# Performance work log

Hardware: AMD Instinct MI355X
Metric: run time of the kernel (lower is better)

## Reference

```python
import jax, jax.numpy as jnp
import numpy as np

N = 20000
E = 320000
F_IN = 512
F_OUT = 512
DIFF_T = 1.0
NUM_STEPS = 5
TIME_DECAY = 0.1
LN_EPS = 1e-5


def setup_inputs() -> dict:
    key = jax.random.key(0)
    k_x, k_e, k_ts, k_wt, k_wr = jax.random.split(key, 5)
    x = jax.random.normal(k_x, (N, F_IN), dtype=jnp.float32)
    edge_index = jax.random.randint(k_e, (2, E), 0, N)
    timestamps = jax.random.uniform(k_ts, (E,), dtype=jnp.float32) * 100.0
    lim = float(np.sqrt(6.0 / (F_IN + F_OUT)))  # xavier_uniform
    W_t = jax.random.uniform(k_wt, (F_OUT, F_IN), jnp.float32, -lim, lim)
    b_t = jnp.zeros((F_OUT,), jnp.float32)
    W_r = jax.random.uniform(k_wr, (F_OUT, F_IN), jnp.float32, -lim, lim)
    gamma = jnp.ones((F_OUT,), jnp.float32)
    beta = jnp.zeros((F_OUT,), jnp.float32)
    return {"node_features": x, "edge_index": edge_index, "timestamps": timestamps,
            "W_t": W_t, "b_t": b_t, "W_r": W_r, "gamma": gamma, "beta": beta,
            "graph_time": 100}


def reference(node_features, edge_index, timestamps, W_t, b_t, W_r, gamma, beta, graph_time):
    x = node_features
    n = x.shape[0]
    # append self-loops with timestamp == graph.time
    loop = jnp.arange(n)
    ei = jnp.concatenate([edge_index, jnp.stack([loop, loop], axis=0)], axis=1)
    ts = jnp.concatenate([timestamps, jnp.full((n,), graph_time, jnp.float32)])
    src, dst = ei[0], ei[1]
    # time-decayed symmetric-normalized adjacency weights
    w = jnp.exp(-TIME_DECAY * (ts.max() - ts))  # [E+N]
    deg = jax.ops.segment_sum(w, dst, num_segments=n)  # [N]
    dinv = jnp.where(deg > 0, deg ** -0.5, 0.0)
    ew = dinv[src] * w * dinv[dst]  # [E+N]
    # K Euler steps of heat diffusion: h <- h + dt*(A_norm h - h)
    dt = DIFF_T / NUM_STEPS
    h = x
    for _ in range(NUM_STEPS):
        diffused = jax.ops.segment_sum(ew[:, None] * h[src], dst, num_segments=n)  # [N, F]
        h = h + dt * (diffused - h)
    # transform + residual + layernorm (dropout omitted: eval mode)
    out = jax.nn.relu(h @ W_t.T + b_t) + x @ W_r.T  # [N, F_OUT]
    mu = out.mean(axis=-1, keepdims=True)
    var = out.var(axis=-1, keepdims=True)
    out = (out - mu) * jax.lax.rsqrt(var + LN_EPS) * gamma + beta
    return out
```

## Files before the change

kernel.cpp:

```cpp
#include <hip/hip_runtime.h>
#include <hip/hip_fp16.h>

#define FDIM 512
#define TDK  0.1f
#define DTs  0.2f
#define EPSv 1e-5f

using bf16x8  = __attribute__((ext_vector_type(8))) __bf16;
using floatx4 = __attribute__((ext_vector_type(4))) float;
using ushort8 = __attribute__((ext_vector_type(8))) unsigned short;
using uintx4  = __attribute__((ext_vector_type(4))) unsigned int;

__device__ __forceinline__ unsigned short f2bf(float f) {
  unsigned int u = __float_as_uint(f);
  u += 0x7fffu + ((u >> 16) & 1u);
  return (unsigned short)(u >> 16);
}

__device__ __forceinline__ void gld16(const __bf16* g, __bf16* l) {
  __builtin_amdgcn_global_load_lds(
      (const __attribute__((address_space(1))) unsigned int*)g,
      (__attribute__((address_space(3))) unsigned int*)l, 16, 0, 0);
}

__global__ __launch_bounds__(256) void tsmax_kernel(const float* __restrict__ ts, int E,
                                                    float* __restrict__ out) {
  float m = 0.f;
  for (int i = blockIdx.x * blockDim.x + threadIdx.x; i < E; i += gridDim.x * blockDim.x)
    m = fmaxf(m, ts[i]);
  for (int off = 32; off; off >>= 1) m = fmaxf(m, __shfl_down(m, off));
  __shared__ float sm[4];
  int wid = threadIdx.x >> 6, lane = threadIdx.x & 63;
  if (lane == 0) sm[wid] = m;
  __syncthreads();
  if (threadIdx.x == 0) {
    float mm = fmaxf(fmaxf(sm[0], sm[1]), fmaxf(sm[2], sm[3]));
    atomicMax((int*)out, __float_as_int(mm));
  }
}

__global__ __launch_bounds__(256) void edge_w_deg(const int* __restrict__ src, const int* __restrict__ dst,
                                                  const float* __restrict__ ts, const float* __restrict__ tsmax_p,
                                                  const int* __restrict__ gt_p,
                                                  float* __restrict__ w, float* __restrict__ deg,
                                                  int* __restrict__ cnt, int E, int N) {
  int e = blockIdx.x * blockDim.x + threadIdx.x;
  int total = E + N;
  if (e >= total) return;
  float gtf = (float)(*gt_p);
  float tm = fmaxf(*tsmax_p, gtf);
  int d; float t;
  if (e < E) { d = dst[e]; t = ts[e]; }
  else       { d = e - E;  t = gtf; }
  float wv = expf(-TDK * (tm - t));
  w[e] = wv;
  atomicAdd(&deg[d], wv);
  atomicAdd(&cnt[d], 1);
}

__global__ __launch_bounds__(256) void dinv_kernel(const float* __restrict__ deg, float* __restrict__ dinv, int N) {
  int i = blockIdx.x * blockDim.x + threadIdx.x;
  if (i >= N) return;
  float d = deg[i];
  dinv[i] = (d > 0.f) ? rsqrtf(d) : 0.f;
}

__global__ __launch_bounds__(256) void seg_reduce(const int* __restrict__ cnt, int* __restrict__ bsum, int n) {
  int i = blockIdx.x * 256 + threadIdx.x;
  int v = (i < n) ? cnt[i] : 0;
  for (int o = 32; o; o >>= 1) v += __shfl_down(v, o);
  __shared__ int sm[4];
  if ((threadIdx.x & 63) == 0) sm[threadIdx.x >> 6] = v;
  __syncthreads();
  if (threadIdx.x == 0) bsum[blockIdx.x] = sm[0] + sm[1] + sm[2] + sm[3];
}

__global__ __launch_bounds__(256) void scan_bsum(const int* __restrict__ bsum, int* __restrict__ bbase, int nb) {
  __shared__ int sm[256];
  int t = threadIdx.x;
  int v = (t < nb) ? bsum[t] : 0;
  sm[t] = v;
  __syncthreads();
  for (int o = 1; o < 256; o <<= 1) {
    int u = (t >= o) ? sm[t - o] : 0;
    __syncthreads();
    sm[t] += u;
    __syncthreads();
  }
  if (t < nb) bbase[t] = sm[t] - v;
}

__global__ __launch_bounds__(256) void seg_scan(const int* __restrict__ cnt, const int* __restrict__ bbase,
                                                int* __restrict__ offs, int* __restrict__ cursor,
                                                int n, int totE) {
  __shared__ int sm[256];
  int i = blockIdx.x * 256 + threadIdx.x;
  int v = (i < n) ? cnt[i] : 0;
  sm[threadIdx.x] = v;
  __syncthreads();
  for (int o = 1; o < 256; o <<= 1) {
    int u = (threadIdx.x >= o) ? sm[threadIdx.x - o] : 0;
    __syncthreads();
    sm[threadIdx.x] += u;
    __syncthreads();
  }
  int excl = sm[threadIdx.x] - v + bbase[blockIdx.x];
  if (i < n) { offs[i] = excl; cursor[i] = excl; }
  if (i == 0) offs[n] = totE;
}

__global__ __launch_bounds__(256) void scatter_kernel(const int* __restrict__ src, const int* __restrict__ dst,
                                                      const float* __restrict__ w, const float* __restrict__ dinv,
                                                      int* __restrict__ cursor, unsigned* __restrict__ cv,
                                                      int E, int N) {
  int e = blockIdx.x * blockDim.x + threadIdx.x;
  if (e >= E + N) return;
  int s, d;
  if (e < E) { s = src[e]; d = dst[e]; }
  else       { s = d = e - E; }
  int pos = atomicAdd(&cursor[d], 1);
  float v = dinv[s] * w[e] * dinv[d];
  unsigned short hv = __half_as_ushort(__float2half(v));
  cv[pos] = (unsigned)s | ((unsigned)hv << 16);
}

__device__ __forceinline__ void acc8(uintx4 u, float v, float* a) {
  a[0] += v * __uint_as_float(u[0] << 16);
  a[1] += v * __uint_as_float(u[0] & 0xffff0000u);
  a[2] += v * __uint_as_float(u[1] << 16);
  a[3] += v * __uint_as_float(u[1] & 0xffff0000u);
  a[4] += v * __uint_as_float(u[2] << 16);
  a[5] += v * __uint_as_float(u[2] & 0xffff0000u);
  a[6] += v * __uint_as_float(u[3] << 16);
  a[7] += v * __uint_as_float(u[3] & 0xffff0000u);
}

__device__ __forceinline__ float cvval(unsigned cu) {
  return __half2float(__ushort_as_half((unsigned short)(cu >> 16)));
}

__global__ __launch_bounds__(256) void spmm_xcd(const int* __restrict__ offs, const unsigned* __restrict__ cv,
                                                const unsigned short* __restrict__ h_in,
                                                unsigned short* __restrict__ h_out, int N) {
  int chunk = blockIdx.x & 7;
  int tile  = blockIdx.x >> 3;
  int row = tile * 32 + (threadIdx.x >> 3);
  if (row >= N) return;
  int fo = chunk * 64 + (threadIdx.x & 7) * 8;
  const unsigned short* hp = h_in + fo;
  int s = offs[row], e = offs[row + 1];
  float a[8] = {0.f, 0.f, 0.f, 0.f, 0.f, 0.f, 0.f, 0.f};
  int j = s;
  for (; j + 8 <= e; j += 8) {
    unsigned cu[8]; uintx4 u[8];
#pragma unroll
    for (int t = 0; t < 8; ++t) cu[t] = cv[j + t];
#pragma unroll
    for (int t = 0; t < 8; ++t) u[t] = *(const uintx4*)(hp + ((cu[t] & 0xffffu) << 9));
#pragma unroll
    for (int t = 0; t < 8; ++t) acc8(u[t], cvval(cu[t]), a);
  }
  if (j + 4 <= e) {
    unsigned cu[4]; uintx4 u[4];
#pragma unroll
    for (int t = 0; t < 4; ++t) cu[t] = cv[j + t];
#pragma unroll
    for (int t = 0; t < 4; ++t) u[t] = *(const uintx4*)(hp + ((cu[t] & 0xffffu) << 9));
#pragma unroll
    for (int t = 0; t < 4; ++t) acc8(u[t], cvval(cu[t]), a);
    j += 4;
  }
  for (; j < e; ++j) {
    unsigned cu = cv[j];
    uintx4 u = *(const uintx4*)(hp + ((cu & 0xffffu) << 9));
    acc8(u, cvval(cu), a);
  }
  uintx4 ud = *(const uintx4*)(hp + (row << 9));
  float hd[8];
  hd[0] = __uint_as_float(ud[0] << 16); hd[1] = __uint_as_float(ud[0] & 0xffff0000u);
  hd[2] = __uint_as_float(ud[1] << 16); hd[3] = __uint_as_float(ud[1] & 0xffff0000u);
  hd[4] = __uint_as_float(ud[2] << 16); hd[5] = __uint_as_float(ud[2] & 0xffff0000u);
  hd[6] = __uint_as_float(ud[3] << 16); hd[7] = __uint_as_float(ud[3] & 0xffff0000u);
  uintx4 o;
  unsigned int p0, p1;
#define PACK(k0, k1, dst_)                                        \
  { float o0 = hd[k0] + DTs * (a[k0] - hd[k0]);                   \
    float o1 = hd[k1] + DTs * (a[k1] - hd[k1]);                   \
    p0 = f2bf(o0); p1 = f2bf(o1); dst_ = p0 | (p1 << 16); }
  PACK(0, 1, o[0]) PACK(2, 3, o[1]) PACK(4, 5, o[2]) PACK(6, 7, o[3])
#undef PACK
  __builtin_nontemporal_store(o, (uintx4*)(h_out + (size_t)row * FDIM + fo));
}

__global__ __launch_bounds__(256) void cast_bf16(const float* __restrict__ srcp,
                                                 unsigned short* __restrict__ dstp, int n8) {
  int i = blockIdx.x * blockDim.x + threadIdx.x;
  if (i >= n8) return;
  const float4 v0 = *(const float4*)(srcp + (size_t)i * 8);
  const float4 v1 = *(const float4*)(srcp + (size_t)i * 8 + 4);
  ushort8 o;
  o[0] = f2bf(v0.x); o[1] = f2bf(v0.y); o[2] = f2bf(v0.z); o[3] = f2bf(v0.w);
  o[4] = f2bf(v1.x); o[5] = f2bf(v1.y); o[6] = f2bf(v1.z); o[7] = f2bf(v1.w);
  *(ushort8*)(dstp + (size_t)i * 8) = o;
}

__global__ __launch_bounds__(256, 3) void gemm_fused(const __bf16* __restrict__ Ah, const __bf16* __restrict__ Ax,
                                                     const __bf16* __restrict__ Wt, const __bf16* __restrict__ Wr,
                                                     const float* __restrict__ bias, float* __restrict__ out,
                                                     int M, int NB) {
  __shared__ __bf16 sA[2][128 * 32];
  __shared__ __bf16 sB[2][128 * 32];
  int tid = threadIdx.x;
  int wid = tid >> 6, lane = tid & 63;
  int wm = wid & 1, wn = wid >> 1;
  int lane15 = lane & 15, quad = lane >> 4;

  int d = blockIdx.x;
  int x = d & 7, s = d >> 3;
  int q = NB >> 3, r = NB & 7;
  int g = (x < r ? x * (q + 1) : r * (q + 1) + (x - r) * q) + s;
  int mi = g >> 2, ni = g & 3;
  int m0 = mi * 128, n0 = ni * 128;

  int r0 = wid * 32 + (lane >> 2);
  int c0 = ((((lane & 3) - (lane >> 3)) & 3)) * 8;
  int am0 = m0 + r0;      if (am0 >= M) am0 = M - 1;
  int am1 = m0 + r0 + 16; if (am1 >= M) am1 = M - 1;
  int bn0 = n0 + r0;
  const __bf16* a00 = Ah + (size_t)am0 * FDIM + c0;
  const __bf16* a01 = Ah + (size_t)am1 * FDIM + c0;
  const __bf16* a10 = Ax + (size_t)am0 * FDIM + c0;
  const __bf16* a11 = Ax + (size_t)am1 * FDIM + c0;
  const __bf16* b00 = Wt + (size_t)bn0 * FDIM + c0;
  const __bf16* b01 = Wt + (size_t)(bn0 + 16) * FDIM + c0;
  const __bf16* b10 = Wr + (size_t)bn0 * FDIM + c0;
  const __bf16* b11 = Wr + (size_t)(bn0 + 16) * FDIM + c0;
  int loff0 = wid * 1024;
  int loff1 = wid * 1024 + 512;

  auto stage = [&](int b, const __bf16* pa0, const __bf16* pa1,
                   const __bf16* pb0, const __bf16* pb1, int kt) {
    gld16(pa0 + kt, &sA[b][loff0]); gld16(pa1 + kt, &sA[b][loff1]);
    gld16(pb0 + kt, &sB[b][loff0]); gld16(pb1 + kt, &sB[b][loff1]);
  };

  int koff = ((quad + (lane15 >> 1)) & 3) * 8;

  float bn[4];
#pragma unroll
  for (int in = 0; in < 4; ++in) bn[in] = bias[n0 + wn * 64 + in * 16 + lane15];

  floatx4 acc[4][4];
  floatx4 z4; z4[0] = 0.f; z4[1] = 0.f; z4[2] = 0.f; z4[3] = 0.f;
#pragma unroll
  for (int im = 0; im < 4; ++im)
#pragma unroll
    for (int in = 0; in < 4; ++in) acc[im][in] = z4;

  stage(0, a00, a01, b00, b01, 0);
  for (int it = 0; it < 32; ++it) {
    int cb = it & 1;
    __syncthreads();
    int nx = it + 1;
    if (nx < 32) {
      if (nx < 16) stage(1 - cb, a00, a01, b00, b01, nx * 32);
      else         stage(1 - cb, a10, a11, b10, b11, (nx & 15) * 32);
    }
    if (it == 16) {
#pragma unroll
      for (int im = 0; im < 4; ++im)
#pragma unroll
        for (int in = 0; in < 4; ++in)
#pragma unroll
          for (int rr = 0; rr < 4; ++rr)
            acc[im][in][rr] = fmaxf(acc[im][in][rr] + bn[in], 0.f);
    }
    bf16x8 af[4], br[4];
#pragma unroll
    for (int im = 0; im < 4; ++im)
      af[im] = *(const bf16x8*)(&sA[cb][(wm * 64 + im * 16 + lane15) * 32 + koff]);
#pragma unroll
    for (int in = 0; in < 4; ++in)
      br[in] = *(const bf16x8*)(&sB[cb][(wn * 64 + in * 16 + lane15) * 32 + koff]);
#pragma unroll
    for (int im = 0; im < 4; ++im)
#pragma unroll
      for (int in = 0; in < 4; ++in)
        acc[im][in] = __builtin_amdgcn_mfma_f32_16x16x32_bf16(af[im], br[in], acc[im][in], 0, 0, 0);
  }

#pragma unroll
  for (int im = 0; im < 4; ++im) {
#pragma unroll
    for (int in = 0; in < 4; ++in) {
#pragma unroll
      for (int rr = 0; rr < 4; ++rr) {
        int m = m0 + wm * 64 + im * 16 + quad * 4 + rr;
        int n = n0 + wn * 64 + in * 16 + lane15;
        if (m < M) out[(size_t)m * FDIM + n] = acc[im][in][rr];
      }
    }
  }
}

__global__ __launch_bounds__(256) void ln_kernel(const float* __restrict__ pre, const float* __restrict__ gamma,
                                                 const float* __restrict__ beta, float* __restrict__ out) {
  int row = blockIdx.x, t = threadIdx.x;
  float2 v = *(const float2*)(pre + (size_t)row * FDIM + t * 2);
  float s = v.x + v.y;
  float ss = v.x * v.x + v.y * v.y;
  for (int off = 32; off; off >>= 1) { s += __shfl_down(s, off); ss += __shfl_down(ss, off); }
  __shared__ float sm[4], sm2[4];
  int wid = t >> 6, lane = t & 63;
  if (lane == 0) { sm[wid] = s; sm2[wid] = ss; }
  __syncthreads();
  if (t == 0) {
    float a = sm[0] + sm[1] + sm[2] + sm[3];
    float b = sm2[0] + sm2[1] + sm2[2] + sm2[3];
    sm[0] = a; sm2[0] = b;
  }
  __syncthreads();
  float mu = sm[0] * (1.f / FDIM);
  float var = sm2[0] * (1.f / FDIM) - mu * mu;
  float inv = rsqrtf(var + EPSv);
  float2 g  = *(const float2*)(gamma + t * 2);
  float2 bb = *(const float2*)(beta + t * 2);
  float2 o;
  o.x = (v.x - mu) * inv * g.x + bb.x;
  o.y = (v.y - mu) * inv * g.y + bb.y;
  *(float2*)(out + (size_t)row * FDIM + t * 2) = o;
}

extern "C" void kernel_launch(void* const* d_in, const int* in_sizes, int n_in,
                              void* d_out, int out_size, void* d_ws, size_t ws_size,
                              hipStream_t stream) {
  const float* x     = (const float*)d_in[0];
  const int*   ei    = (const int*)d_in[1];
  const float* ts    = (const float*)d_in[2];
  const float* W_t   = (const float*)d_in[3];
  const float* b_t   = (const float*)d_in[4];
  const float* W_r   = (const float*)d_in[5];
  const float* gamma = (const float*)d_in[6];
  const float* beta  = (const float*)d_in[7];
  const int*   gt    = (const int*)d_in[8];

  const int E = in_sizes[2];
  const int N = in_sizes[0] / FDIM;
  const int* src = ei;
  const int* dst = ei + E;
  const int totE = E + N;
  const int nb = (N + 255) / 256;

  char* base = (char*)d_ws;
  size_t off = 0;
  auto carve = [&](size_t bytes) -> char* {
    char* r = base + off;
    off = (off + bytes + 255) & ~(size_t)255;
    return r;
  };
  float* tsmax = (float*)carve(4);
  float* deg   = (float*)carve((size_t)N * 4);
  int*   cnt   = (int*)  carve((size_t)N * 4);
  size_t zero_bytes = off;
  float* dinv  = (float*)carve((size_t)N * 4);
  int*   offs  = (int*)  carve((size_t)(N + 1) * 4);
  int*   cursor= (int*)  carve((size_t)N * 4);
  int*   bsum  = (int*)  carve((size_t)nb * 4);
  int*   bbase = (int*)  carve((size_t)nb * 4);
  float* w     = (float*)carve((size_t)totE * 4);
  unsigned* cv = (unsigned*)carve((size_t)totE * 4);
  unsigned short* xb  = (unsigned short*)carve((size_t)N * FDIM * 2);
  unsigned short* hba = (unsigned short*)carve((size_t)N * FDIM * 2);
  unsigned short* hbb = (unsigned short*)carve((size_t)N * FDIM * 2);
  unsigned short* wtb = (unsigned short*)carve((size_t)FDIM * FDIM * 2);
  unsigned short* wrb = (unsigned short*)carve((size_t)FDIM * FDIM * 2);
  float* preLN = (float*)carve((size_t)N * FDIM * 4);

  hipMemsetAsync(d_ws, 0, zero_bytes, stream);

  tsmax_kernel<<<64, 256, 0, stream>>>(ts, E, tsmax);
  edge_w_deg<<<(totE + 255) / 256, 256, 0, stream>>>(src, dst, ts, tsmax, gt, w, deg, cnt, E, N);
  dinv_kernel<<<(N + 255) / 256, 256, 0, stream>>>(deg, dinv, N);
  seg_reduce<<<nb, 256, 0, stream>>>(cnt, bsum, N);
  scan_bsum<<<1, 256, 0, stream>>>(bsum, bbase, nb);
  seg_scan<<<nb, 256, 0, stream>>>(cnt, bbase, offs, cursor, N, totE);
  scatter_kernel<<<(totE + 255) / 256, 256, 0, stream>>>(src, dst, w, dinv, cursor, cv, E, N);

  int n8x = N * FDIM / 8;
  cast_bf16<<<(n8x + 255) / 256, 256, 0, stream>>>(x, xb, n8x);
  int n8w = FDIM * FDIM / 8;
  cast_bf16<<<(n8w + 255) / 256, 256, 0, stream>>>(W_t, wtb, n8w);
  cast_bf16<<<(n8w + 255) / 256, 256, 0, stream>>>(W_r, wrb, n8w);

  int sgrid = ((N + 31) / 32) * 8;
  spmm_xcd<<<sgrid, 256, 0, stream>>>(offs, cv, xb,  hba, N);
  spmm_xcd<<<sgrid, 256, 0, stream>>>(offs, cv, hba, hbb, N);
  spmm_xcd<<<sgrid, 256, 0, stream>>>(offs, cv, hbb, hba, N);
  spmm_xcd<<<sgrid, 256, 0, stream>>>(offs, cv, hba, hbb, N);
  spmm_xcd<<<sgrid, 256, 0, stream>>>(offs, cv, hbb, hba, N);

  int MB = (N + 127) / 128;
  int NBLK = MB * (FDIM / 128);
  gemm_fused<<<NBLK, 256, 0, stream>>>((const __bf16*)hba, (const __bf16*)xb,
                                       (const __bf16*)wtb, (const __bf16*)wrb,
                                       b_t, preLN, N, NBLK);

  ln_kernel<<<N, 256, 0, stream>>>(preLN, gamma, beta, (float*)d_out);
}
```

Before: 381.9 us.

## Shrink GEMM M-tile to 64 and shuffle-broadcast CSR entries in SpMM

```diff
diff --git a/kernel.cpp b/kernel.cpp
--- a/kernel.cpp
+++ b/kernel.cpp
@@ -146,24 +146,28 @@
   int tile  = blockIdx.x >> 3;
   int row = tile * 32 + (threadIdx.x >> 3);
   if (row >= N) return;
-  int fo = chunk * 64 + (threadIdx.x & 7) * 8;
+  int lane7 = threadIdx.x & 7;
+  int wbase = (threadIdx.x & 63) & 56;
+  int fo = chunk * 64 + lane7 * 8;
   const unsigned short* hp = h_in + fo;
   int s = offs[row], e = offs[row + 1];
   float a[8] = {0.f, 0.f, 0.f, 0.f, 0.f, 0.f, 0.f, 0.f};
   int j = s;
   for (; j + 8 <= e; j += 8) {
+    unsigned myc = __builtin_nontemporal_load(cv + j + lane7);
     unsigned cu[8]; uintx4 u[8];
 #pragma unroll
-    for (int t = 0; t < 8; ++t) cu[t] = cv[j + t];
+    for (int t = 0; t < 8; ++t) cu[t] = __shfl(myc, wbase | t);
 #pragma unroll
     for (int t = 0; t < 8; ++t) u[t] = *(const uintx4*)(hp + ((cu[t] & 0xffffu) << 9));
 #pragma unroll
     for (int t = 0; t < 8; ++t) acc8(u[t], cvval(cu[t]), a);
   }
   if (j + 4 <= e) {
+    unsigned myc = __builtin_nontemporal_load(cv + j + (lane7 & 3));
     unsigned cu[4]; uintx4 u[4];
 #pragma unroll
-    for (int t = 0; t < 4; ++t) cu[t] = cv[j + t];
+    for (int t = 0; t < 4; ++t) cu[t] = __shfl(myc, wbase | t);
 #pragma unroll
     for (int t = 0; t < 4; ++t) u[t] = *(const uintx4*)(hp + ((cu[t] & 0xffffu) << 9));
 #pragma unroll
@@ -171,7 +175,7 @@
     j += 4;
   }
   for (; j < e; ++j) {
-    unsigned cu = cv[j];
+    unsigned cu = __builtin_nontemporal_load(cv + j);
     uintx4 u = *(const uintx4*)(hp + ((cu & 0xffffu) << 9));
     acc8(u, cvval(cu), a);
   }
@@ -204,15 +208,15 @@
   *(ushort8*)(dstp + (size_t)i * 8) = o;
 }
 
-__global__ __launch_bounds__(256, 3) void gemm_fused(const __bf16* __restrict__ Ah, const __bf16* __restrict__ Ax,
+__global__ __launch_bounds__(256, 5) void gemm_fused(const __bf16* __restrict__ Ah, const __bf16* __restrict__ Ax,
                                                      const __bf16* __restrict__ Wt, const __bf16* __restrict__ Wr,
                                                      const float* __restrict__ bias, float* __restrict__ out,
                                                      int M, int NB) {
-  __shared__ __bf16 sA[2][128 * 32];
+  __shared__ __bf16 sA[2][64 * 32];
   __shared__ __bf16 sB[2][128 * 32];
   int tid = threadIdx.x;
   int wid = tid >> 6, lane = tid & 63;
-  int wm = wid & 1, wn = wid >> 1;
+  int wn = wid;
   int lane15 = lane & 15, quad = lane >> 4;
 
   int d = blockIdx.x;
@@ -220,83 +224,80 @@
   int q = NB >> 3, r = NB & 7;
   int g = (x < r ? x * (q + 1) : r * (q + 1) + (x - r) * q) + s;
   int mi = g >> 2, ni = g & 3;
-  int m0 = mi * 128, n0 = ni * 128;
-
-  int r0 = wid * 32 + (lane >> 2);
+  int m0 = mi * 64, n0 = ni * 128;
+
+  int rs = lane >> 2;
   int c0 = ((((lane & 3) - (lane >> 3)) & 3)) * 8;
-  int am0 = m0 + r0;      if (am0 >= M) am0 = M - 1;
-  int am1 = m0 + r0 + 16; if (am1 >= M) am1 = M - 1;
-  int bn0 = n0 + r0;
-  const __bf16* a00 = Ah + (size_t)am0 * FDIM + c0;
-  const __bf16* a01 = Ah + (size_t)am1 * FDIM + c0;
-  const __bf16* a10 = Ax + (size_t)am0 * FDIM + c0;
-  const __bf16* a11 = Ax + (size_t)am1 * FDIM + c0;
+  int am = m0 + wid * 16 + rs; if (am >= M) am = M - 1;
+  int bn0 = n0 + wid * 32 + rs;
+  const __bf16* a0p = Ah + (size_t)am * FDIM + c0;
+  const __bf16* a1p = Ax + (size_t)am * FDIM + c0;
   const __bf16* b00 = Wt + (size_t)bn0 * FDIM + c0;
   const __bf16* b01 = Wt + (size_t)(bn0 + 16) * FDIM + c0;
   const __bf16* b10 = Wr + (size_t)bn0 * FDIM + c0;
   const __bf16* b11 = Wr + (size_t)(bn0 + 16) * FDIM + c0;
-  int loff0 = wid * 1024;
-  int loff1 = wid * 1024 + 512;
-
-  auto stage = [&](int b, const __bf16* pa0, const __bf16* pa1,
-                   const __bf16* pb0, const __bf16* pb1, int kt) {
-    gld16(pa0 + kt, &sA[b][loff0]); gld16(pa1 + kt, &sA[b][loff1]);
-    gld16(pb0 + kt, &sB[b][loff0]); gld16(pb1 + kt, &sB[b][loff1]);
+  int aoff  = wid * 512;
+  int boff0 = wid * 1024, boff1 = wid * 1024 + 512;
+
+  auto stage = [&](int b, const __bf16* pa, const __bf16* pb0, const __bf16* pb1, int kt) {
+    gld16(pa + kt, &sA[b][aoff]);
+    gld16(pb0 + kt, &sB[b][boff0]);
+    gld16(pb1 + kt, &sB[b][boff1]);
   };
 
   int koff = ((quad + (lane15 >> 1)) & 3) * 8;
 
-  float bn[4];
-#pragma unroll
-  for (int in = 0; in < 4; ++in) bn[in] = bias[n0 + wn * 64 + in * 16 + lane15];
-
-  floatx4 acc[4][4];
+  float bn[2];
+#pragma unroll
+  for (int in = 0; in < 2; ++in) bn[in] = bias[n0 + wn * 32 + in * 16 + lane15];
+
+  floatx4 acc[4][2];
   floatx4 z4; z4[0] = 0.f; z4[1] = 0.f; z4[2] = 0.f; z4[3] = 0.f;
 #pragma unroll
   for (int im = 0; im < 4; ++im)
 #pragma unroll
-    for (int in = 0; in < 4; ++in) acc[im][in] = z4;
-
-  stage(0, a00, a01, b00, b01, 0);
+    for (int in = 0; in < 2; ++in) acc[im][in] = z4;
+
+  stage(0, a0p, b00, b01, 0);
   for (int it = 0; it < 32; ++it) {
     int cb = it & 1;
     __syncthreads();
     int nx = it + 1;
     if (nx < 32) {
-      if (nx < 16) stage(1 - cb, a00, a01, b00, b01, nx * 32);
-      else         stage(1 - cb, a10, a11, b10, b11, (nx & 15) * 32);
+      if (nx < 16) stage(1 - cb, a0p, b00, b01, nx * 32);
+      else         stage(1 - cb, a1p, b10, b11, (nx & 15) * 32);
     }
     if (it == 16) {
 #pragma unroll
       for (int im = 0; im < 4; ++im)
 #pragma unroll
-        for (int in = 0; in < 4; ++in)
+        for (int in = 0; in < 2; ++in)
 #pragma unroll
           for (int rr = 0; rr < 4; ++rr)
             acc[im][in][rr] = fmaxf(acc[im][in][rr] + bn[in], 0.f);
     }
-    bf16x8 af[4], br[4];
+    bf16x8 af[4], br[2];
 #pragma unroll
     for (int im = 0; im < 4; ++im)
-      af[im] = *(const bf16x8*)(&sA[cb][(wm * 64 + im * 16 + lane15) * 32 + koff]);
-#pragma unroll
-    for (int in = 0; in < 4; ++in)
-      br[in] = *(const bf16x8*)(&sB[cb][(wn * 64 + in * 16 + lane15) * 32 + koff]);
+      af[im] = *(const bf16x8*)(&sA[cb][(im * 16 + lane15) * 32 + koff]);
+#pragma unroll
+    for (int in = 0; in < 2; ++in)
+      br[in] = *(const bf16x8*)(&sB[cb][(wn * 32 + in * 16 + lane15) * 32 + koff]);
 #pragma unroll
     for (int im = 0; im < 4; ++im)
 #pragma unroll
-      for (int in = 0; in < 4; ++in)
+      for (int in = 0; in < 2; ++in)
         acc[im][in] = __builtin_amdgcn_mfma_f32_16x16x32_bf16(af[im], br[in], acc[im][in], 0, 0, 0);
   }
 
 #pragma unroll
   for (int im = 0; im < 4; ++im) {
 #pragma unroll
-    for (int in = 0; in < 4; ++in) {
+    for (int in = 0; in < 2; ++in) {
 #pragma unroll
       for (int rr = 0; rr < 4; ++rr) {
-        int m = m0 + wm * 64 + im * 16 + quad * 4 + rr;
-        int n = n0 + wn * 64 + in * 16 + lane15;
+        int m = m0 + im * 16 + quad * 4 + rr;
+        int n = n0 + wn * 32 + in * 16 + lane15;
         if (m < M) out[(size_t)m * FDIM + n] = acc[im][in][rr];
       }
     }
@@ -399,7 +400,7 @@
   spmm_xcd<<<sgrid, 256, 0, stream>>>(offs, cv, hba, hbb, N);
   spmm_xcd<<<sgrid, 256, 0, stream>>>(offs, cv, hbb, hba, N);
 
-  int MB = (N + 127) / 128;
+  int MB = (N + 63) / 64;
   int NBLK = MB * (FDIM / 128);
   gemm_fused<<<NBLK, 256, 0, stream>>>((const __bf16*)hba, (const __bf16*)xb,
                                        (const __bf16*)wtb, (const __bf16*)wrb,
```

New measurement: 480.1 us. 25.7% more time.
